# Kernel tuning notes

Measured on AMD Instinct MI355X. Metric: run time of the kernel, lower is better.

The kernel has to match this reference:

```python
import jax, jax.numpy as jnp
import numpy as np

N_NODES = 500_000
N_EDGES = 8_000_000
N_GRAPHS = 25_000
NUM_TASKS = 138
READOUT_DIM = 175
MLP_DIMS = (96, 63)
BN_EPS = 1e-5


def _linear_params(key, fan_in, fan_out):
    k1, k2 = jax.random.split(key)
    bound = 1.0 / np.sqrt(fan_in)
    W = jax.random.uniform(k1, (fan_in, fan_out), jnp.float32, -bound, bound)
    b = jax.random.uniform(k2, (fan_out,), jnp.float32, -bound, bound)
    return W, b


def setup_inputs() -> dict:
    key = jax.random.key(0)
    ks = jax.random.split(key, 16)
    inp = {}
    inp["x"] = jax.random.normal(ks[0], (N_NODES, 48), jnp.float32)
    inp["mol_features"] = jax.random.normal(ks[1], (N_GRAPHS, 10), jnp.float32)
    inp["edge_index"] = jax.random.randint(ks[2], (2, N_EDGES), 0, N_NODES, jnp.int32)
    inp["batch"] = jnp.sort(jax.random.randint(ks[3], (N_NODES,), 0, N_GRAPHS, jnp.int32))
    # GCN layer linears (message transform)
    inp["w_g1"], inp["b_g1"] = _linear_params(ks[4], 48, 20)
    inp["w_g2"], inp["b_g2"] = _linear_params(ks[5], 20, 27)
    inp["w_g3"], inp["b_g3"] = _linear_params(ks[6], 27, 36)
    inp["w_g4"], inp["b_g4"] = _linear_params(ks[7], 36, 36)
    # Readout linears
    inp["w_r1"], inp["b_r1"] = _linear_params(ks[8], 20, READOUT_DIM)
    inp["w_r2"], inp["b_r2"] = _linear_params(ks[9], 27, READOUT_DIM)
    inp["w_r3"], inp["b_r3"] = _linear_params(ks[10], 36, READOUT_DIM)
    inp["w_r4"], inp["b_r4"] = _linear_params(ks[11], 36, READOUT_DIM)
    # MLP
    inp["w_fc1"], inp["b_fc1"] = _linear_params(ks[12], READOUT_DIM + 10, MLP_DIMS[0])
    inp["bn1_g"] = jnp.ones((MLP_DIMS[0],), jnp.float32)
    inp["bn1_b"] = jnp.zeros((MLP_DIMS[0],), jnp.float32)
    inp["w_fc2"], inp["b_fc2"] = _linear_params(ks[13], MLP_DIMS[0], MLP_DIMS[1])
    inp["bn2_g"] = jnp.ones((MLP_DIMS[1],), jnp.float32)
    inp["bn2_b"] = jnp.zeros((MLP_DIMS[1],), jnp.float32)
    inp["w_out"], inp["b_out"] = _linear_params(ks[14], MLP_DIMS[1], NUM_TASKS)
    return inp


def _gcn(x, src, dst, W, b):
    # message: Linear on gathered source features; aggregate: scatter-max; update: SELU
    m = x[src] @ W + b                                  # [E, out]
    agg = jax.ops.segment_max(m, dst, num_segments=N_NODES)
    agg = jnp.where(jnp.isfinite(agg), agg, 0.0)        # PyG fills empty segments with 0
    return jax.nn.selu(agg)


def _readout(x, batch, W, b):
    return jax.ops.segment_sum(x, batch, num_segments=N_GRAPHS) @ W + b


def _bn(h, g, b):
    mu = h.mean(axis=0)
    var = h.var(axis=0)
    return g * (h - mu) / jnp.sqrt(var + BN_EPS) + b


def reference(x, mol_features, w_g1, b_g1, w_g2, b_g2, w_g3, b_g3, w_g4, b_g4,
              w_r1, b_r1, w_r2, b_r2, w_r3, b_r3, w_r4, b_r4,
              w_fc1, b_fc1, bn1_g, bn1_b, w_fc2, b_fc2, bn2_g, bn2_b,
              w_out, b_out, edge_index, batch):
    src, dst = edge_index[0], edge_index[1]
    x1 = _gcn(x, src, dst, w_g1, b_g1)
    x2 = _gcn(x1, src, dst, w_g2, b_g2)
    x3 = _gcn(x2, src, dst, w_g3, b_g3)
    x4 = _gcn(x3, src, dst, w_g4, b_g4)
    r = (_readout(x1, batch, w_r1, b_r1) + _readout(x2, batch, w_r2, b_r2)
         + _readout(x3, batch, w_r3, b_r3) + _readout(x4, batch, w_r4, b_r4))
    h = jnp.concatenate([r, mol_features], axis=1)      # [G, 185]
    h = jax.nn.relu(_bn(h @ w_fc1 + b_fc1, bn1_g, bn1_b))
    h = jax.nn.relu(_bn(h @ w_fc2 + b_fc2, bn2_g, bn2_b))
    return jax.nn.sigmoid(h @ w_out + b_out)            # [G, num_tasks]
```

## Files before the change

### kernel.cpp

```cpp
#include <hip/hip_runtime.h>
#include <hip/hip_fp16.h>
#include <math.h>

#define N_NODES  500000
#define N_EDGES  8000000
#define N_GRAPHS 25000
#define SD  119
#define RD  175
#define H1  96
#define H2  63
#define NT  138
#define GPB 16

#define B2SHIFT 11
#define B2NODES 2048
#define NBUCK2  245
#define REG     40960
#define BIN_CHUNK 4096
#define NB_BIN 1954
#define NBF 7813
#define CSR_CAP 1536

static __device__ __forceinline__ float selu_f(float m){
    const float scale=1.0507009873554805f, alpha=1.6732632423543772f;
    return m > 0.0f ? scale*m : scale*alpha*(__expf(m)-1.0f);
}

static __device__ __forceinline__ unsigned pkmax(unsigned a, unsigned b){
    unsigned r;
    asm volatile("v_pk_max_f16 %0, %1, %2" : "=v"(r) : "v"(a), "v"(b));
    return r;
}

static __device__ __forceinline__ float2 h2_to_f2(unsigned u){
    union{ unsigned u; __half2 h; } c; c.u = u;
    return __half22float2(c.h);
}

struct __align__(8) U4 { unsigned x, y, z, w; };

static __device__ __forceinline__ int wave_incl_scan(int v){
    int lane = threadIdx.x & 63;
    #pragma unroll
    for(int off=1; off<64; off<<=1){
        int u = __shfl_up(v, off, 64);
        if(lane >= off) v += u;
    }
    return v;
}

__global__ void k_init(int* bcur, float* S){
    int i = blockIdx.x*256 + threadIdx.x;
    if(i < NBUCK2) bcur[i] = i*REG;
    if(i < N_GRAPHS*SD) S[i] = 0.f;
}

__global__ __launch_bounds__(256) void k_bin(const int* __restrict__ src, const int* __restrict__ dst,
                                             int* __restrict__ bcur, int* __restrict__ packed){
    __shared__ int   stage[BIN_CHUNK];
    __shared__ unsigned char bkt[BIN_CHUNK];
    __shared__ int lhist[256], lstart[256], lcur[256], gbase[256];
    __shared__ int wsum[4];
    int t = threadIdx.x;
    int base = blockIdx.x*BIN_CHUNK;
    int myb[16], mys[16];
    #pragma unroll
    for(int k=0;k<16;k++){
        int e = base + k*256 + t;
        if(e < N_EDGES){
            int d = dst[e];
            myb[k] = d >> B2SHIFT;
            mys[k] = ((d & (B2NODES-1)) << 19) | src[e];
        } else myb[k] = -1;
    }
    lhist[t]=0; __syncthreads();
    #pragma unroll
    for(int k=0;k<16;k++) if(myb[k]>=0) atomicAdd(&lhist[myb[k]],1);
    __syncthreads();
    int v = lhist[t];
    int incl = wave_incl_scan(v);
    if((t&63)==63) wsum[t>>6] = incl;
    __syncthreads();
    int wbase = 0;
    for(int w=0; w<(t>>6); w++) wbase += wsum[w];
    int exc = wbase + incl - v;
    lstart[t]=exc; lcur[t]=exc;
    if(t < NBUCK2 && v>0) gbase[t] = atomicAdd(&bcur[t], v);
    __syncthreads();
    #pragma unroll
    for(int k=0;k<16;k++){
        if(myb[k]>=0){
            int p = atomicAdd(&lcur[myb[k]],1);
            stage[p]=mys[k]; bkt[p]=(unsigned char)myb[k];
        }
    }
    __syncthreads();
    int total = N_EDGES - base; if(total > BIN_CHUNK) total = BIN_CHUNK;
    for(int i=t; i<total; i+=256){
        int b = bkt[i];
        packed[gbase[b] + (i - lstart[b])] = stage[i];
    }
}

__global__ __launch_bounds__(1024) void k_scatfine(const int* __restrict__ bcur,
                          const int* __restrict__ packed, int* __restrict__ row_beg,
                          int* __restrict__ row_end, int* __restrict__ csr){
    __shared__ int cnt[B2NODES];
    __shared__ int wsum[16];
    int t = threadIdx.x;
    int b = blockIdx.x;
    int nb = b << B2SHIFT;
    cnt[t]=0; cnt[t+1024]=0;
    __syncthreads();
    int ebeg = b*REG, eend = bcur[b];
    for(int e=ebeg+t; e<eend; e+=1024){
        int dl = packed[e] >> 19;
        atomicAdd(&cnt[dl],1);
    }
    __syncthreads();
    int c0 = cnt[2*t], c1 = cnt[2*t+1];
    int s = c0+c1;
    int incl = wave_incl_scan(s);
    if((t&63)==63) wsum[t>>6] = incl;
    __syncthreads();
    int wbase=0;
    for(int w=0; w<(t>>6); w++) wbase += wsum[w];
    int excl = wbase + incl - s;
    int e0 = excl, e1 = excl + c0;
    cnt[2*t]=e0; cnt[2*t+1]=e1;
    int n0 = nb + 2*t, n1 = nb + 2*t + 1;
    if(n0 < N_NODES){ row_beg[n0]=ebeg+e0; row_end[n0]=ebeg+e0+c0; }
    if(n1 < N_NODES){ row_beg[n1]=ebeg+e1; row_end[n1]=ebeg+e1+c1; }
    __syncthreads();
    for(int e=ebeg+t; e<eend; e+=1024){
        int v = packed[e];
        int dl = v >> 19;
        int pos = ebeg + atomicAdd(&cnt[dl],1);
        csr[pos] = v & 0x7FFFF;
    }
}

template<int DIN,int DOUT,int PIN,int PH>
__global__ __launch_bounds__(256) void k_transform_h(const float* __restrict__ x, const float* __restrict__ W,
                                                     const float* __restrict__ bias, __half* __restrict__ y){
    __shared__ float swp[PIN*PH];
    __shared__ float sbp[PH];
    int t = threadIdx.x;
    for(int i=t;i<PIN*PH;i+=256){
        int row=i/PH, o=i-row*PH;
        swp[i] = (row<DIN && o<DOUT) ? W[row*DOUT+o] : 0.f;
    }
    if(t<PH) sbp[t] = (t<DOUT) ? bias[t] : 0.f;
    __syncthreads();
    const int TPN = PH/2;
    int gid = blockIdx.x*256 + t;
    if(gid >= N_NODES*TPN) return;
    int n = gid/TPN, op = gid - n*TPN;
    int o0 = 2*op, o1 = o0+1;
    const float4* xr4 = (const float4*)(x + (size_t)n*PIN);
    float acc0 = sbp[o0], acc1 = sbp[o1];
    #pragma unroll
    for(int i4=0;i4<PIN/4;i4++){
        float4 xv = xr4[i4];
        acc0 = fmaf(xv.x, swp[(4*i4+0)*PH+o0], acc0);
        acc1 = fmaf(xv.x, swp[(4*i4+0)*PH+o1], acc1);
        acc0 = fmaf(xv.y, swp[(4*i4+1)*PH+o0], acc0);
        acc1 = fmaf(xv.y, swp[(4*i4+1)*PH+o1], acc1);
        acc0 = fmaf(xv.z, swp[(4*i4+2)*PH+o0], acc0);
        acc1 = fmaf(xv.z, swp[(4*i4+2)*PH+o1], acc1);
        acc0 = fmaf(xv.w, swp[(4*i4+3)*PH+o0], acc0);
        acc1 = fmaf(xv.w, swp[(4*i4+3)*PH+o1], acc1);
    }
    __half2* y2 = (__half2*)y;
    y2[(size_t)n*TPN + op] = __floats2half2_rn(acc0, acc1);
}

template<int ROWB, class IDX>
static __device__ __forceinline__ void gather_max(const __half* __restrict__ yin,
        IDX idx, int beg, int end, unsigned offb, unsigned m[4]){
    const char* __restrict__ yb = (const char*)yin;
    unsigned m0=m[0], m1=m[1], m2=m[2], m3=m[3];
    int j = beg;
    for(; j+8<=end; j+=8){
        int s0=idx(j+0), s1=idx(j+1), s2=idx(j+2), s3=idx(j+3);
        int s4=idx(j+4), s5=idx(j+5), s6=idx(j+6), s7=idx(j+7);
        U4 v0 = *(const U4*)(yb + ((unsigned)s0*(unsigned)ROWB + offb));
        U4 v1 = *(const U4*)(yb + ((unsigned)s1*(unsigned)ROWB + offb));
        U4 v2 = *(const U4*)(yb + ((unsigned)s2*(unsigned)ROWB + offb));
        U4 v3 = *(const U4*)(yb + ((unsigned)s3*(unsigned)ROWB + offb));
        U4 v4 = *(const U4*)(yb + ((unsigned)s4*(unsigned)ROWB + offb));
        U4 v5 = *(const U4*)(yb + ((unsigned)s5*(unsigned)ROWB + offb));
        U4 v6 = *(const U4*)(yb + ((unsigned)s6*(unsigned)ROWB + offb));
        U4 v7 = *(const U4*)(yb + ((unsigned)s7*(unsigned)ROWB + offb));
        m0=pkmax(m0,v0.x); m1=pkmax(m1,v0.y); m2=pkmax(m2,v0.z); m3=pkmax(m3,v0.w);
        m0=pkmax(m0,v1.x); m1=pkmax(m1,v1.y); m2=pkmax(m2,v1.z); m3=pkmax(m3,v1.w);
        m0=pkmax(m0,v2.x); m1=pkmax(m1,v2.y); m2=pkmax(m2,v2.z); m3=pkmax(m3,v2.w);
        m0=pkmax(m0,v3.x); m1=pkmax(m1,v3.y); m2=pkmax(m2,v3.z); m3=pkmax(m3,v3.w);
        m0=pkmax(m0,v4.x); m1=pkmax(m1,v4.y); m2=pkmax(m2,v4.z); m3=pkmax(m3,v4.w);
        m0=pkmax(m0,v5.x); m1=pkmax(m1,v5.y); m2=pkmax(m2,v5.z); m3=pkmax(m3,v5.w);
        m0=pkmax(m0,v6.x); m1=pkmax(m1,v6.y); m2=pkmax(m2,v6.z); m3=pkmax(m3,v6.w);
        m0=pkmax(m0,v7.x); m1=pkmax(m1,v7.y); m2=pkmax(m2,v7.z); m3=pkmax(m3,v7.w);
    }
    for(; j+4<=end; j+=4){
        int s0=idx(j+0), s1=idx(j+1), s2=idx(j+2), s3=idx(j+3);
        U4 v0 = *(const U4*)(yb + ((unsigned)s0*(unsigned)ROWB + offb));
        U4 v1 = *(const U4*)(yb + ((unsigned)s1*(unsigned)ROWB + offb));
        U4 v2 = *(const U4*)(yb + ((unsigned)s2*(unsigned)ROWB + offb));
        U4 v3 = *(const U4*)(yb + ((unsigned)s3*(unsigned)ROWB + offb));
        m0=pkmax(m0,v0.x); m1=pkmax(m1,v0.y); m2=pkmax(m2,v0.z); m3=pkmax(m3,v0.w);
        m0=pkmax(m0,v1.x); m1=pkmax(m1,v1.y); m2=pkmax(m2,v1.z); m3=pkmax(m3,v1.w);
        m0=pkmax(m0,v2.x); m1=pkmax(m1,v2.y); m2=pkmax(m2,v2.z); m3=pkmax(m3,v2.w);
        m0=pkmax(m0,v3.x); m1=pkmax(m1,v3.y); m2=pkmax(m2,v3.z); m3=pkmax(m3,v3.w);
    }
    for(; j<end; j++){
        int s0 = idx(j);
        U4 v0 = *(const U4*)(yb + ((unsigned)s0*(unsigned)ROWB + offb));
        m0=pkmax(m0,v0.x); m1=pkmax(m1,v0.y); m2=pkmax(m2,v0.z); m3=pkmax(m3,v0.w);
    }
    m[0]=m0; m[1]=m1; m[2]=m2; m[3]=m3;
}

static __device__ __forceinline__ void finish_selu(const unsigned m[4], float o[8]){
    float2 f0=h2_to_f2(m[0]), f1=h2_to_f2(m[1]), f2=h2_to_f2(m[2]), f3=h2_to_f2(m[3]);
    float f[8] = {f0.x,f0.y,f1.x,f1.y,f2.x,f2.y,f3.x,f3.y};
    #pragma unroll
    for(int k=0;k<8;k++){
        float v = f[k];
        if(v < -1e30f) v = 0.0f;
        o[k] = selu_f(v);
    }
}

template<int ROWB_IN,int D_CUR,int SOFF,int D_NEXT,int ROWB_NEXT>
__global__ __launch_bounds__(64*(ROWB_IN/16+1)) void k_fused(
        const __half* __restrict__ yin, const int* __restrict__ row_beg,
        const int* __restrict__ row_end, const int* __restrict__ csr,
        const int* __restrict__ batch,
        const float* __restrict__ W, const float* __restrict__ bias,
        float* __restrict__ S, __half* __restrict__ yout){
    const int FG  = ROWB_IN/16 + 1;
    const int NTH = 64*FG;
    const int NF  = ROWB_IN/2;
    const int OH  = ROWB_NEXT/2;
    __shared__ float feat[64][NF+1];
    __shared__ float sw[D_CUR*OH];
    __shared__ float sb[OH];
    __shared__ int sbatch[64];
    __shared__ int scsr[CSR_CAP];
    int t = threadIdx.x;
    int nl = t / FG, fg = t - nl*FG;
    int base = blockIdx.x*64;
    int n = base + nl;
    for(int i=t;i<D_CUR*OH;i+=NTH){
        int k=i/OH, o2=i-k*OH;
        sw[i] = (o2<D_NEXT) ? W[k*D_NEXT+o2] : 0.f;
    }
    if(t<OH) sb[t] = (t<D_NEXT) ? bias[t] : 0.f;
    if(t<64) sbatch[t] = (base+t<N_NODES) ? batch[base+t] : -1;
    int last = base + 63; if(last >= N_NODES) last = N_NODES-1;
    int ebeg = row_beg[base];
    int nst = row_end[last] - ebeg; if(nst > CSR_CAP) nst = CSR_CAP;
    for(int i=t;i<nst;i+=NTH) scsr[i] = csr[ebeg+i];
    __syncthreads();
    int slim = ebeg + nst;
    unsigned offb = (unsigned)(fg*16 < ROWB_IN-16 ? fg*16 : ROWB_IN-16);
    float o[8];
    if(n < N_NODES){
        int beg = row_beg[n], end = row_end[n];
        unsigned m[4] = {0xFC00FC00u,0xFC00FC00u,0xFC00FC00u,0xFC00FC00u};
        if(end <= slim) gather_max<ROWB_IN>(yin, [&](int j){ return scsr[j-ebeg]; }, beg, end, offb, m);
        else            gather_max<ROWB_IN>(yin, [&](int j){ return csr[j]; },       beg, end, offb, m);
        finish_selu(m, o);
    } else {
        for(int k=0;k<8;k++) o[k]=0.f;
    }
    int offh = (int)(offb>>1);
    #pragma unroll
    for(int k=0;k<8;k++) feat[nl][offh+k] = o[k];
    __syncthreads();
    if(t < D_CUR){
        float acc=0.f; int gprev = sbatch[0];
        for(int mm=0;mm<64;mm++){
            int g = sbatch[mm];
            if(g<0) break;
            if(g!=gprev){ atomicAdd(&S[(size_t)gprev*SD+SOFF+t], acc); acc=0.f; gprev=g; }
            acc += feat[mm][t];
        }
        if(gprev>=0) atomicAdd(&S[(size_t)gprev*SD+SOFF+t], acc);
    }
    if(n < N_NODES){
        for(int o2=fg; o2<OH/2; o2+=FG){
            int c0=2*o2, c1=c0+1;
            float a0=sb[c0], a1=sb[c1];
            #pragma unroll
            for(int k=0;k<D_CUR;k++){
                float fv = feat[nl][k];
                a0 = fmaf(fv, sw[k*OH+c0], a0);
                a1 = fmaf(fv, sw[k*OH+c1], a1);
            }
            ((__half2*)yout)[(size_t)n*(OH/2)+o2] = __floats2half2_rn(a0,a1);
        }
    }
}

template<int ROWB_IN,int D_CUR,int SOFF>
__global__ __launch_bounds__(64*(ROWB_IN/16+1)) void k_fused_last(
        const __half* __restrict__ yin, const int* __restrict__ row_beg,
        const int* __restrict__ row_end, const int* __restrict__ csr,
        const int* __restrict__ batch, float* __restrict__ S){
    const int FG  = ROWB_IN/16 + 1;
    const int NTH = 64*FG;
    const int NF  = ROWB_IN/2;
    __shared__ float feat[64][NF+1];
    __shared__ int sbatch[64];
    __shared__ int scsr[CSR_CAP];
    int t = threadIdx.x;
    int nl = t / FG, fg = t - nl*FG;
    int base = blockIdx.x*64;
    int n = base + nl;
    if(t<64) sbatch[t] = (base+t<N_NODES) ? batch[base+t] : -1;
    int last = base + 63; if(last >= N_NODES) last = N_NODES-1;
    int ebeg = row_beg[base];
    int nst = row_end[last] - ebeg; if(nst > CSR_CAP) nst = CSR_CAP;
    for(int i=t;i<nst;i+=NTH) scsr[i] = csr[ebeg+i];
    __syncthreads();
    int slim = ebeg + nst;
    unsigned offb = (unsigned)(fg*16 < ROWB_IN-16 ? fg*16 : ROWB_IN-16);
    float o[8];
    if(n < N_NODES){
        int beg = row_beg[n], end = row_end[n];
        unsigned m[4] = {0xFC00FC00u,0xFC00FC00u,0xFC00FC00u,0xFC00FC00u};
        if(end <= slim) gather_max<ROWB_IN>(yin, [&](int j){ return scsr[j-ebeg]; }, beg, end, offb, m);
        else            gather_max<ROWB_IN>(yin, [&](int j){ return csr[j]; },       beg, end, offb, m);
        finish_selu(m, o);
    } else {
        for(int k=0;k<8;k++) o[k]=0.f;
    }
    int offh = (int)(offb>>1);
    #pragma unroll
    for(int k=0;k<8;k++) feat[nl][offh+k] = o[k];
    __syncthreads();
    if(t < D_CUR){
        float acc=0.f; int gprev = sbatch[0];
        for(int mm=0;mm<64;mm++){
            int g = sbatch[mm];
            if(g<0) break;
            if(g!=gprev){ atomicAdd(&S[(size_t)gprev*SD+SOFF+t], acc); acc=0.f; gprev=g; }
            acc += feat[mm][t];
        }
        if(gprev>=0) atomicAdd(&S[(size_t)gprev*SD+SOFF+t], acc);
    }
}

__global__ __launch_bounds__(192) void k_readout(const float* __restrict__ S,
    const float* __restrict__ w1,const float* __restrict__ b1,
    const float* __restrict__ w2,const float* __restrict__ b2,
    const float* __restrict__ w3,const float* __restrict__ b3,
    const float* __restrict__ w4,const float* __restrict__ b4,
    float* __restrict__ r){
    __shared__ float sH[GPB][SD];
    int t = threadIdx.x;
    int g0 = blockIdx.x*GPB;
    for(int i=t;i<GPB*SD;i+=192){
        int gl=i/SD, k=i-gl*SD;
        int g=g0+gl;
        sH[gl][k] = (g<N_GRAPHS) ? S[(size_t)g*SD+k] : 0.f;
    }
    __syncthreads();
    int j = t;
    if(j < RD){
        float acc[GPB];
        float bj = b1[j]+b2[j]+b3[j]+b4[j];
        #pragma unroll
        for(int gl=0;gl<GPB;gl++) acc[gl]=bj;
        for(int k=0;k<20;k++){ float wv=w1[k*RD+j];
            #pragma unroll
            for(int gl=0;gl<GPB;gl++) acc[gl] += sH[gl][k]*wv; }
        for(int k=0;k<27;k++){ float wv=w2[k*RD+j];
            #pragma unroll
            for(int gl=0;gl<GPB;gl++) acc[gl] += sH[gl][20+k]*wv; }
        for(int k=0;k<36;k++){ float wv=w3[k*RD+j];
            #pragma unroll
            for(int gl=0;gl<GPB;gl++) acc[gl] += sH[gl][47+k]*wv; }
        for(int k=0;k<36;k++){ float wv=w4[k*RD+j];
            #pragma unroll
            for(int gl=0;gl<GPB;gl++) acc[gl] += sH[gl][83+k]*wv; }
        int ng = min(GPB, N_GRAPHS-g0);
        for(int gl=0;gl<ng;gl++) r[(size_t)(g0+gl)*RD+j] = acc[gl];
    }
}

__global__ __launch_bounds__(128) void k_fc1(const float* __restrict__ r, const float* __restrict__ mol,
    const float* __restrict__ w, const float* __restrict__ b,
    float* __restrict__ z1, float* __restrict__ ps, float* __restrict__ pq){
    __shared__ float sH[GPB][RD+10];
    int t = threadIdx.x;
    int g0 = blockIdx.x*GPB;
    for(int i=t;i<GPB*(RD+10);i+=128){
        int gl=i/(RD+10), k=i-gl*(RD+10);
        int g=g0+gl;
        float v=0.f;
        if(g<N_GRAPHS) v = (k<RD) ? r[(size_t)g*RD+k] : mol[(size_t)g*10 + (k-RD)];
        sH[gl][k]=v;
    }
    __syncthreads();
    int j = t;
    if(j < H1){
        float acc[GPB]; float bj=b[j];
        #pragma unroll
        for(int gl=0;gl<GPB;gl++) acc[gl]=bj;
        for(int k=0;k<RD+10;k++){
            float wv = w[k*H1+j];
            #pragma unroll
            for(int gl=0;gl<GPB;gl++) acc[gl] += sH[gl][k]*wv;
        }
        int ng = min(GPB, N_GRAPHS-g0);
        float psum=0.f, psq=0.f;
        for(int gl=0;gl<ng;gl++){
            z1[(size_t)(g0+gl)*H1+j]=acc[gl];
            psum+=acc[gl]; psq+=acc[gl]*acc[gl];
        }
        ps[blockIdx.x*H1+j]=psum;
        pq[blockIdx.x*H1+j]=psq;
    }
}

__global__ __launch_bounds__(256) void k_bnfin(const float* __restrict__ ps, const float* __restrict__ pq,
    int nb, int H, const float* __restrict__ gamma, const float* __restrict__ beta,
    float* __restrict__ a, float* __restrict__ c){
    int j = blockIdx.x;
    int t = threadIdx.x;
    float s=0.f, q=0.f;
    for(int i=t;i<nb;i+=256){ s+=ps[(size_t)i*H+j]; q+=pq[(size_t)i*H+j]; }
    __shared__ float sh1[256], sh2[256];
    sh1[t]=s; sh2[t]=q; __syncthreads();
    for(int off=128;off>0;off>>=1){
        if(t<off){ sh1[t]+=sh1[t+off]; sh2[t]+=sh2[t+off]; }
        __syncthreads();
    }
    if(t==0){
        float mean = sh1[0]/(float)N_GRAPHS;
        float var  = sh2[0]/(float)N_GRAPHS - mean*mean;
        float inv  = 1.0f/sqrtf(var + 1e-5f);
        float aj = gamma[j]*inv;
        a[j]=aj; c[j]=beta[j]-aj*mean;
    }
}

__global__ __launch_bounds__(64) void k_fc2(const float* __restrict__ z1, const float* __restrict__ a1,
    const float* __restrict__ c1, const float* __restrict__ w, const float* __restrict__ b,
    float* __restrict__ z2, float* __restrict__ ps, float* __restrict__ pq){
    __shared__ float sH[GPB][H1];
    int t = threadIdx.x;
    int g0 = blockIdx.x*GPB;
    for(int i=t;i<GPB*H1;i+=64){
        int gl=i/H1, k=i-gl*H1;
        int g=g0+gl;
        float v=0.f;
        if(g<N_GRAPHS){ float z=z1[(size_t)g*H1+k]; v=fmaxf(a1[k]*z+c1[k],0.f); }
        sH[gl][k]=v;
    }
    __syncthreads();
    int j = t;
    if(j < H2){
        float acc[GPB]; float bj=b[j];
        #pragma unroll
        for(int gl=0;gl<GPB;gl++) acc[gl]=bj;
        for(int k=0;k<H1;k++){
            float wv=w[k*H2+j];
            #pragma unroll
            for(int gl=0;gl<GPB;gl++) acc[gl]+=sH[gl][k]*wv;
        }
        int ng=min(GPB,N_GRAPHS-g0);
        float psum=0.f,psq=0.f;
        for(int gl=0;gl<ng;gl++){
            z2[(size_t)(g0+gl)*H2+j]=acc[gl];
            psum+=acc[gl]; psq+=acc[gl]*acc[gl];
        }
        ps[blockIdx.x*H2+j]=psum; pq[blockIdx.x*H2+j]=psq;
    }
}

__global__ __launch_bounds__(192) void k_out(const float* __restrict__ z2, const float* __restrict__ a2,
    const float* __restrict__ c2, const float* __restrict__ w, const float* __restrict__ b,
    float* __restrict__ out){
    __shared__ float sH[GPB][H2];
    int t = threadIdx.x;
    int g0 = blockIdx.x*GPB;
    for(int i=t;i<GPB*H2;i+=192){
        int gl=i/H2, k=i-gl*H2;
        int g=g0+gl;
        float v=0.f;
        if(g<N_GRAPHS){ float z=z2[(size_t)g*H2+k]; v=fmaxf(a2[k]*z+c2[k],0.f); }
        sH[gl][k]=v;
    }
    __syncthreads();
    int j = t;
    if(j < NT){
        float acc[GPB]; float bj=b[j];
        #pragma unroll
        for(int gl=0;gl<GPB;gl++) acc[gl]=bj;
        for(int k=0;k<H2;k++){
            float wv=w[k*NT+j];
            #pragma unroll
            for(int gl=0;gl<GPB;gl++) acc[gl]+=sH[gl][k]*wv;
        }
        int ng=min(GPB,N_GRAPHS-g0);
        for(int gl=0;gl<ng;gl++)
            out[(size_t)(g0+gl)*NT+j] = 1.0f/(1.0f+__expf(-acc[gl]));
    }
}

static inline int ceil_div(int a,int b){ return (a+b-1)/b; }

extern "C" void kernel_launch(void* const* d_in, const int* in_sizes, int n_in,
                              void* d_out, int out_size, void* d_ws, size_t ws_size,
                              hipStream_t stream) {
    const float* x     = (const float*)d_in[0];
    const float* mol   = (const float*)d_in[1];
    const int*   ei    = (const int*)  d_in[2];
    const int*   batch = (const int*)  d_in[3];
    const float* w_g1=(const float*)d_in[4];  const float* b_g1=(const float*)d_in[5];
    const float* w_g2=(const float*)d_in[6];  const float* b_g2=(const float*)d_in[7];
    const float* w_g3=(const float*)d_in[8];  const float* b_g3=(const float*)d_in[9];
    const float* w_g4=(const float*)d_in[10]; const float* b_g4=(const float*)d_in[11];
    const float* w_r1=(const float*)d_in[12]; const float* b_r1=(const float*)d_in[13];
    const float* w_r2=(const float*)d_in[14]; const float* b_r2=(const float*)d_in[15];
    const float* w_r3=(const float*)d_in[16]; const float* b_r3=(const float*)d_in[17];
    const float* w_r4=(const float*)d_in[18]; const float* b_r4=(const float*)d_in[19];
    const float* w_fc1=(const float*)d_in[20]; const float* b_fc1=(const float*)d_in[21];
    const float* bn1_g=(const float*)d_in[22]; const float* bn1_b=(const float*)d_in[23];
    const float* w_fc2=(const float*)d_in[24]; const float* b_fc2=(const float*)d_in[25];
    const float* bn2_g=(const float*)d_in[26]; const float* bn2_b=(const float*)d_in[27];
    const float* w_out=(const float*)d_in[28]; const float* b_out=(const float*)d_in[29];
    float* out = (float*)d_out;

    char* p = (char*)d_ws;
    auto take=[&](size_t bytes)->char*{ char* q=p; p += (bytes+255)&~(size_t)255; return q; };
    __half* yA = (__half*)take((size_t)N_NODES*72 + 256);
    __half* yB = (__half*)take((size_t)N_NODES*72 + 256);
    int* bcur    = (int*)take((size_t)NBUCK2*4);
    int* row_beg = (int*)take((size_t)N_NODES*4);
    int* row_end = (int*)take((size_t)N_NODES*4);
    int* packed  = (int*)take((size_t)NBUCK2*REG*4);
    int* csr     = (int*)take((size_t)NBUCK2*REG*4);
    float* S  = (float*)take((size_t)N_GRAPHS*SD*4);
    float* r  = (float*)take((size_t)N_GRAPHS*RD*4);
    float* z1 = (float*)take((size_t)N_GRAPHS*H1*4);
    float* z2 = (float*)take((size_t)N_GRAPHS*H2*4);
    const int NB_G = ceil_div(N_GRAPHS, GPB);
    float* p1s=(float*)take((size_t)NB_G*H1*4);
    float* p1q=(float*)take((size_t)NB_G*H1*4);
    float* p2s=(float*)take((size_t)NB_G*H2*4);
    float* p2q=(float*)take((size_t)NB_G*H2*4);
    float* a1=(float*)take(H1*4); float* c1=(float*)take(H1*4);
    float* a2=(float*)take(H2*4); float* c2=(float*)take(H2*4);

    const int* src = ei;
    const int* dst = ei + N_EDGES;

    k_init<<<ceil_div(N_GRAPHS*SD,256),256,0,stream>>>(bcur,S);
    k_bin<<<NB_BIN,256,0,stream>>>(src,dst,bcur,packed);
    k_scatfine<<<NBUCK2,1024,0,stream>>>(bcur,packed,row_beg,row_end,csr);

    k_transform_h<48,20,48,20><<<ceil_div(N_NODES*10,256),256,0,stream>>>(x,w_g1,b_g1,yA);
    k_fused<40,20,0, 27,56><<<NBF,192,0,stream>>>(yA,row_beg,row_end,csr,batch,w_g2,b_g2,S,yB);
    k_fused<56,27,20,36,72><<<NBF,256,0,stream>>>(yB,row_beg,row_end,csr,batch,w_g3,b_g3,S,yA);
    k_fused<72,36,47,36,72><<<NBF,320,0,stream>>>(yA,row_beg,row_end,csr,batch,w_g4,b_g4,S,yB);
    k_fused_last<72,36,83><<<NBF,320,0,stream>>>(yB,row_beg,row_end,csr,batch,S);

    k_readout<<<NB_G,192,0,stream>>>(S,w_r1,b_r1,w_r2,b_r2,w_r3,b_r3,w_r4,b_r4,r);
    k_fc1<<<NB_G,128,0,stream>>>(r,mol,w_fc1,b_fc1,z1,p1s,p1q);
    k_bnfin<<<H1,256,0,stream>>>(p1s,p1q,NB_G,H1,bn1_g,bn1_b,a1,c1);
    k_fc2<<<NB_G,64,0,stream>>>(z1,a1,c1,w_fc2,b_fc2,z2,p2s,p2q);
    k_bnfin<<<H2,256,0,stream>>>(p2s,p2q,NB_G,H2,bn2_g,bn2_b,a2,c2);
    k_out<<<NB_G,192,0,stream>>>(z2,a2,c2,w_out,b_out,out);
}
```

Measured before the change: 1.387 ms.

## Split 72-byte node rows into 64-byte main and 8-byte tail arrays

Fp16 node feature rows are now split into a 64-byte main array, which is cache-line aligned and gathered with four 16-byte lanes, and a separate 8-byte tail array for features 32-35. A new tail-gather kernel runs the max/SELU over the tail for the 36-wide layers and writes float4 results that the fused kernel reads. The aim is to avoid 72-byte rows straddling cache lines, which wastes gather bandwidth. In exchange there are two extra edge-traversal kernel launches that reread the CSR indices, and the first layer's padding grows from 40 to 64 bytes.

```diff
diff --git a/kernel.cpp b/kernel.cpp
--- a/kernel.cpp
+++ b/kernel.cpp
@@ -36,8 +36,6 @@
     union{ unsigned u; __half2 h; } c; c.u = u;
     return __half22float2(c.h);
 }
-
-struct __align__(8) U4 { unsigned x, y, z, w; };
 
 static __device__ __forceinline__ int wave_incl_scan(int v){
     int lane = threadIdx.x & 63;
@@ -175,23 +173,23 @@
     y2[(size_t)n*TPN + op] = __floats2half2_rn(acc0, acc1);
 }
 
-template<int ROWB, class IDX>
-static __device__ __forceinline__ void gather_max(const __half* __restrict__ yin,
+template<class IDX>
+static __device__ __forceinline__ void gather_max_m(const __half* __restrict__ ymain,
         IDX idx, int beg, int end, unsigned offb, unsigned m[4]){
-    const char* __restrict__ yb = (const char*)yin;
+    const char* __restrict__ yb = (const char*)ymain;
     unsigned m0=m[0], m1=m[1], m2=m[2], m3=m[3];
     int j = beg;
     for(; j+8<=end; j+=8){
         int s0=idx(j+0), s1=idx(j+1), s2=idx(j+2), s3=idx(j+3);
         int s4=idx(j+4), s5=idx(j+5), s6=idx(j+6), s7=idx(j+7);
-        U4 v0 = *(const U4*)(yb + ((unsigned)s0*(unsigned)ROWB + offb));
-        U4 v1 = *(const U4*)(yb + ((unsigned)s1*(unsigned)ROWB + offb));
-        U4 v2 = *(const U4*)(yb + ((unsigned)s2*(unsigned)ROWB + offb));
-        U4 v3 = *(const U4*)(yb + ((unsigned)s3*(unsigned)ROWB + offb));
-        U4 v4 = *(const U4*)(yb + ((unsigned)s4*(unsigned)ROWB + offb));
-        U4 v5 = *(const U4*)(yb + ((unsigned)s5*(unsigned)ROWB + offb));
-        U4 v6 = *(const U4*)(yb + ((unsigned)s6*(unsigned)ROWB + offb));
-        U4 v7 = *(const U4*)(yb + ((unsigned)s7*(unsigned)ROWB + offb));
+        uint4 v0 = *(const uint4*)(yb + ((unsigned)s0*64u + offb));
+        uint4 v1 = *(const uint4*)(yb + ((unsigned)s1*64u + offb));
+        uint4 v2 = *(const uint4*)(yb + ((unsigned)s2*64u + offb));
+        uint4 v3 = *(const uint4*)(yb + ((unsigned)s3*64u + offb));
+        uint4 v4 = *(const uint4*)(yb + ((unsigned)s4*64u + offb));
+        uint4 v5 = *(const uint4*)(yb + ((unsigned)s5*64u + offb));
+        uint4 v6 = *(const uint4*)(yb + ((unsigned)s6*64u + offb));
+        uint4 v7 = *(const uint4*)(yb + ((unsigned)s7*64u + offb));
         m0=pkmax(m0,v0.x); m1=pkmax(m1,v0.y); m2=pkmax(m2,v0.z); m3=pkmax(m3,v0.w);
         m0=pkmax(m0,v1.x); m1=pkmax(m1,v1.y); m2=pkmax(m2,v1.z); m3=pkmax(m3,v1.w);
         m0=pkmax(m0,v2.x); m1=pkmax(m1,v2.y); m2=pkmax(m2,v2.z); m3=pkmax(m3,v2.w);
@@ -203,10 +201,10 @@
     }
     for(; j+4<=end; j+=4){
         int s0=idx(j+0), s1=idx(j+1), s2=idx(j+2), s3=idx(j+3);
-        U4 v0 = *(const U4*)(yb + ((unsigned)s0*(unsigned)ROWB + offb));
-        U4 v1 = *(const U4*)(yb + ((unsigned)s1*(unsigned)ROWB + offb));
-        U4 v2 = *(const U4*)(yb + ((unsigned)s2*(unsigned)ROWB + offb));
-        U4 v3 = *(const U4*)(yb + ((unsigned)s3*(unsigned)ROWB + offb));
+        uint4 v0 = *(const uint4*)(yb + ((unsigned)s0*64u + offb));
+        uint4 v1 = *(const uint4*)(yb + ((unsigned)s1*64u + offb));
+        uint4 v2 = *(const uint4*)(yb + ((unsigned)s2*64u + offb));
+        uint4 v3 = *(const uint4*)(yb + ((unsigned)s3*64u + offb));
         m0=pkmax(m0,v0.x); m1=pkmax(m1,v0.y); m2=pkmax(m2,v0.z); m3=pkmax(m3,v0.w);
         m0=pkmax(m0,v1.x); m1=pkmax(m1,v1.y); m2=pkmax(m2,v1.z); m3=pkmax(m3,v1.w);
         m0=pkmax(m0,v2.x); m1=pkmax(m1,v2.y); m2=pkmax(m2,v2.z); m3=pkmax(m3,v2.w);
@@ -214,7 +212,7 @@
     }
     for(; j<end; j++){
         int s0 = idx(j);
-        U4 v0 = *(const U4*)(yb + ((unsigned)s0*(unsigned)ROWB + offb));
+        uint4 v0 = *(const uint4*)(yb + ((unsigned)s0*64u + offb));
         m0=pkmax(m0,v0.x); m1=pkmax(m1,v0.y); m2=pkmax(m2,v0.z); m3=pkmax(m3,v0.w);
     }
     m[0]=m0; m[1]=m1; m[2]=m2; m[3]=m3;
@@ -231,31 +229,64 @@
     }
 }
 
-template<int ROWB_IN,int D_CUR,int SOFF,int D_NEXT,int ROWB_NEXT>
-__global__ __launch_bounds__(64*(ROWB_IN/16+1)) void k_fused(
-        const __half* __restrict__ yin, const int* __restrict__ row_beg,
-        const int* __restrict__ row_end, const int* __restrict__ csr,
-        const int* __restrict__ batch,
+__global__ __launch_bounds__(256) void k_tailgather(const __half* __restrict__ ytail,
+        const int* __restrict__ row_beg, const int* __restrict__ row_end,
+        const int* __restrict__ csr, float* __restrict__ tf){
+    int n = blockIdx.x*256 + threadIdx.x;
+    if(n >= N_NODES) return;
+    const char* __restrict__ yb = (const char*)ytail;
+    int beg = row_beg[n], end = row_end[n];
+    unsigned m0=0xFC00FC00u, m1=0xFC00FC00u;
+    int j = beg;
+    for(; j+4<=end; j+=4){
+        int s0=csr[j], s1=csr[j+1], s2=csr[j+2], s3=csr[j+3];
+        uint2 v0 = *(const uint2*)(yb + (unsigned)s0*8u);
+        uint2 v1 = *(const uint2*)(yb + (unsigned)s1*8u);
+        uint2 v2 = *(const uint2*)(yb + (unsigned)s2*8u);
+        uint2 v3 = *(const uint2*)(yb + (unsigned)s3*8u);
+        m0=pkmax(m0,v0.x); m1=pkmax(m1,v0.y);
+        m0=pkmax(m0,v1.x); m1=pkmax(m1,v1.y);
+        m0=pkmax(m0,v2.x); m1=pkmax(m1,v2.y);
+        m0=pkmax(m0,v3.x); m1=pkmax(m1,v3.y);
+    }
+    for(; j<end; j++){
+        uint2 v0 = *(const uint2*)(yb + (unsigned)csr[j]*8u);
+        m0=pkmax(m0,v0.x); m1=pkmax(m1,v0.y);
+    }
+    float2 f0=h2_to_f2(m0), f1=h2_to_f2(m1);
+    float4 o;
+    o.x = (f0.x < -1e30f) ? 0.f : f0.x;
+    o.y = (f0.y < -1e30f) ? 0.f : f0.y;
+    o.z = (f1.x < -1e30f) ? 0.f : f1.x;
+    o.w = (f1.y < -1e30f) ? 0.f : f1.y;
+    o.x = selu_f(o.x); o.y = selu_f(o.y); o.z = selu_f(o.z); o.w = selu_f(o.w);
+    ((float4*)tf)[n] = o;
+}
+
+template<int FG,int TIN,int D_CUR,int SOFF,int D_NEXT,int TNEXT>
+__global__ __launch_bounds__(64*FG) void k_fused(
+        const __half* __restrict__ ymain, const float* __restrict__ tf,
+        const int* __restrict__ row_beg, const int* __restrict__ row_end,
+        const int* __restrict__ csr, const int* __restrict__ batch,
         const float* __restrict__ W, const float* __restrict__ bias,
-        float* __restrict__ S, __half* __restrict__ yout){
-    const int FG  = ROWB_IN/16 + 1;
+        float* __restrict__ S, __half* __restrict__ youtM, __half* __restrict__ youtT){
     const int NTH = 64*FG;
-    const int NF  = ROWB_IN/2;
-    const int OH  = ROWB_NEXT/2;
+    const int NF  = TIN ? 36 : 8*FG;
+    const int OW  = TNEXT ? 36 : 32;
     __shared__ float feat[64][NF+1];
-    __shared__ float sw[D_CUR*OH];
-    __shared__ float sb[OH];
+    __shared__ float sw[D_CUR*OW];
+    __shared__ float sb[OW];
     __shared__ int sbatch[64];
     __shared__ int scsr[CSR_CAP];
     int t = threadIdx.x;
     int nl = t / FG, fg = t - nl*FG;
     int base = blockIdx.x*64;
     int n = base + nl;
-    for(int i=t;i<D_CUR*OH;i+=NTH){
-        int k=i/OH, o2=i-k*OH;
+    for(int i=t;i<D_CUR*OW;i+=NTH){
+        int k=i/OW, o2=i-k*OW;
         sw[i] = (o2<D_NEXT) ? W[k*D_NEXT+o2] : 0.f;
     }
-    if(t<OH) sb[t] = (t<D_NEXT) ? bias[t] : 0.f;
+    if(t<OW) sb[t] = (t<D_NEXT) ? bias[t] : 0.f;
     if(t<64) sbatch[t] = (base+t<N_NODES) ? batch[base+t] : -1;
     int last = base + 63; if(last >= N_NODES) last = N_NODES-1;
     int ebeg = row_beg[base];
@@ -263,20 +294,27 @@
     for(int i=t;i<nst;i+=NTH) scsr[i] = csr[ebeg+i];
     __syncthreads();
     int slim = ebeg + nst;
-    unsigned offb = (unsigned)(fg*16 < ROWB_IN-16 ? fg*16 : ROWB_IN-16);
     float o[8];
     if(n < N_NODES){
         int beg = row_beg[n], end = row_end[n];
         unsigned m[4] = {0xFC00FC00u,0xFC00FC00u,0xFC00FC00u,0xFC00FC00u};
-        if(end <= slim) gather_max<ROWB_IN>(yin, [&](int j){ return scsr[j-ebeg]; }, beg, end, offb, m);
-        else            gather_max<ROWB_IN>(yin, [&](int j){ return csr[j]; },       beg, end, offb, m);
+        unsigned offb = (unsigned)fg*16u;
+        if(end <= slim) gather_max_m(ymain, [&](int j){ return scsr[j-ebeg]; }, beg, end, offb, m);
+        else            gather_max_m(ymain, [&](int j){ return csr[j]; },       beg, end, offb, m);
         finish_selu(m, o);
     } else {
         for(int k=0;k<8;k++) o[k]=0.f;
     }
-    int offh = (int)(offb>>1);
-    #pragma unroll
-    for(int k=0;k<8;k++) feat[nl][offh+k] = o[k];
+    #pragma unroll
+    for(int k=0;k<8;k++) feat[nl][8*fg+k] = o[k];
+    if(TIN && fg == 0){
+        if(n < N_NODES){
+            float4 tv = ((const float4*)tf)[n];
+            feat[nl][32]=tv.x; feat[nl][33]=tv.y; feat[nl][34]=tv.z; feat[nl][35]=tv.w;
+        } else {
+            feat[nl][32]=0.f; feat[nl][33]=0.f; feat[nl][34]=0.f; feat[nl][35]=0.f;
+        }
+    }
     __syncthreads();
     if(t < D_CUR){
         float acc=0.f; int gprev = sbatch[0];
@@ -289,28 +327,30 @@
         if(gprev>=0) atomicAdd(&S[(size_t)gprev*SD+SOFF+t], acc);
     }
     if(n < N_NODES){
-        for(int o2=fg; o2<OH/2; o2+=FG){
-            int c0=2*o2, c1=c0+1;
+        for(int p=fg; p<OW/2; p+=FG){
+            int c0=2*p, c1=c0+1;
             float a0=sb[c0], a1=sb[c1];
             #pragma unroll
             for(int k=0;k<D_CUR;k++){
                 float fv = feat[nl][k];
-                a0 = fmaf(fv, sw[k*OH+c0], a0);
-                a1 = fmaf(fv, sw[k*OH+c1], a1);
+                a0 = fmaf(fv, sw[k*OW+c0], a0);
+                a1 = fmaf(fv, sw[k*OW+c1], a1);
             }
-            ((__half2*)yout)[(size_t)n*(OH/2)+o2] = __floats2half2_rn(a0,a1);
-        }
-    }
-}
-
-template<int ROWB_IN,int D_CUR,int SOFF>
-__global__ __launch_bounds__(64*(ROWB_IN/16+1)) void k_fused_last(
-        const __half* __restrict__ yin, const int* __restrict__ row_beg,
-        const int* __restrict__ row_end, const int* __restrict__ csr,
-        const int* __restrict__ batch, float* __restrict__ S){
-    const int FG  = ROWB_IN/16 + 1;
+            __half2 hv = __floats2half2_rn(a0,a1);
+            if(!TNEXT || p < 16) ((__half2*)youtM)[(size_t)n*16 + p] = hv;
+            else                 ((__half2*)youtT)[(size_t)n*2 + (p-16)] = hv;
+        }
+    }
+}
+
+template<int FG,int TIN,int D_CUR,int SOFF>
+__global__ __launch_bounds__(64*FG) void k_fused_last(
+        const __half* __restrict__ ymain, const float* __restrict__ tf,
+        const int* __restrict__ row_beg, const int* __restrict__ row_end,
+        const int* __restrict__ csr, const int* __restrict__ batch,
+        float* __restrict__ S){
     const int NTH = 64*FG;
-    const int NF  = ROWB_IN/2;
+    const int NF  = TIN ? 36 : 8*FG;
     __shared__ float feat[64][NF+1];
     __shared__ int sbatch[64];
     __shared__ int scsr[CSR_CAP];
@@ -325,20 +365,27 @@
     for(int i=t;i<nst;i+=NTH) scsr[i] = csr[ebeg+i];
     __syncthreads();
     int slim = ebeg + nst;
-    unsigned offb = (unsigned)(fg*16 < ROWB_IN-16 ? fg*16 : ROWB_IN-16);
     float o[8];
     if(n < N_NODES){
         int beg = row_beg[n], end = row_end[n];
         unsigned m[4] = {0xFC00FC00u,0xFC00FC00u,0xFC00FC00u,0xFC00FC00u};
-        if(end <= slim) gather_max<ROWB_IN>(yin, [&](int j){ return scsr[j-ebeg]; }, beg, end, offb, m);
-        else            gather_max<ROWB_IN>(yin, [&](int j){ return csr[j]; },       beg, end, offb, m);
+        unsigned offb = (unsigned)fg*16u;
+        if(end <= slim) gather_max_m(ymain, [&](int j){ return scsr[j-ebeg]; }, beg, end, offb, m);
+        else            gather_max_m(ymain, [&](int j){ return csr[j]; },       beg, end, offb, m);
         finish_selu(m, o);
     } else {
         for(int k=0;k<8;k++) o[k]=0.f;
     }
-    int offh = (int)(offb>>1);
-    #pragma unroll
-    for(int k=0;k<8;k++) feat[nl][offh+k] = o[k];
+    #pragma unroll
+    for(int k=0;k<8;k++) feat[nl][8*fg+k] = o[k];
+    if(TIN && fg == 0){
+        if(n < N_NODES){
+            float4 tv = ((const float4*)tf)[n];
+            feat[nl][32]=tv.x; feat[nl][33]=tv.y; feat[nl][34]=tv.z; feat[nl][35]=tv.w;
+        } else {
+            feat[nl][32]=0.f; feat[nl][33]=0.f; feat[nl][34]=0.f; feat[nl][35]=0.f;
+        }
+    }
     __syncthreads();
     if(t < D_CUR){
         float acc=0.f; int gprev = sbatch[0];
@@ -537,8 +584,11 @@
 
     char* p = (char*)d_ws;
     auto take=[&](size_t bytes)->char*{ char* q=p; p += (bytes+255)&~(size_t)255; return q; };
-    __half* yA = (__half*)take((size_t)N_NODES*72 + 256);
-    __half* yB = (__half*)take((size_t)N_NODES*72 + 256);
+    __half* yAm = (__half*)take((size_t)N_NODES*64);
+    __half* yBm = (__half*)take((size_t)N_NODES*64);
+    __half* yAt = (__half*)take((size_t)N_NODES*8);
+    __half* yBt = (__half*)take((size_t)N_NODES*8);
+    float* tf   = (float*)take((size_t)N_NODES*16);
     int* bcur    = (int*)take((size_t)NBUCK2*4);
     int* row_beg = (int*)take((size_t)N_NODES*4);
     int* row_end = (int*)take((size_t)N_NODES*4);
@@ -563,11 +613,13 @@
     k_bin<<<NB_BIN,256,0,stream>>>(src,dst,bcur,packed);
     k_scatfine<<<NBUCK2,1024,0,stream>>>(bcur,packed,row_beg,row_end,csr);
 
-    k_transform_h<48,20,48,20><<<ceil_div(N_NODES*10,256),256,0,stream>>>(x,w_g1,b_g1,yA);
-    k_fused<40,20,0, 27,56><<<NBF,192,0,stream>>>(yA,row_beg,row_end,csr,batch,w_g2,b_g2,S,yB);
-    k_fused<56,27,20,36,72><<<NBF,256,0,stream>>>(yB,row_beg,row_end,csr,batch,w_g3,b_g3,S,yA);
-    k_fused<72,36,47,36,72><<<NBF,320,0,stream>>>(yA,row_beg,row_end,csr,batch,w_g4,b_g4,S,yB);
-    k_fused_last<72,36,83><<<NBF,320,0,stream>>>(yB,row_beg,row_end,csr,batch,S);
+    k_transform_h<48,20,48,32><<<ceil_div(N_NODES*16,256),256,0,stream>>>(x,w_g1,b_g1,yAm);
+    k_fused<3,0,20,0, 27,0><<<NBF,192,0,stream>>>(yAm,tf,row_beg,row_end,csr,batch,w_g2,b_g2,S,yBm,yBt);
+    k_fused<4,0,27,20,36,1><<<NBF,256,0,stream>>>(yBm,tf,row_beg,row_end,csr,batch,w_g3,b_g3,S,yAm,yAt);
+    k_tailgather<<<ceil_div(N_NODES,256),256,0,stream>>>(yAt,row_beg,row_end,csr,tf);
+    k_fused<4,1,36,47,36,1><<<NBF,256,0,stream>>>(yAm,tf,row_beg,row_end,csr,batch,w_g4,b_g4,S,yBm,yBt);
+    k_tailgather<<<ceil_div(N_NODES,256),256,0,stream>>>(yBt,row_beg,row_end,csr,tf);
+    k_fused_last<4,1,36,83><<<NBF,256,0,stream>>>(yBm,tf,row_beg,row_end,csr,batch,S);
 
     k_readout<<<NB_G,192,0,stream>>>(S,w_r1,b_r1,w_r2,b_r2,w_r3,b_r3,w_r4,b_r4,r);
     k_fc1<<<NB_G,128,0,stream>>>(r,mol,w_fc1,b_fc1,z1,p1s,p1q);
```

Result: no change. 1.386 ms (-0.1%).
